# Optimization experiments

Hardware: AMD Instinct MI355X
Metric: run time of the kernel (lower is better)

## Reference

```python
import jax, jax.numpy as jnp
import numpy as np

GAMMA = 0.5
ITERATIONS = 1


def setup_inputs() -> dict:
    key = jax.random.key(0)
    # x: [batch, heads, num_windows, N, dim]
    x = jax.random.normal(key, (4, 8, 64, 256, 128), dtype=jnp.float32)
    return {"x": x}


def _l2norm(v):
    return v / jnp.linalg.norm(v, axis=-1, keepdims=True)


def _get_codebook(x):
    # x: [b,h,w,n,d] -> c: [b,h,w,d]
    B, H, W, N, D = x.shape
    c = _l2norm(jnp.sum(x, axis=-2))              # init: window mean direction
    xf = x.reshape(B, H, W * N, D)                # flatten windows: [b,h,l,d], l = W*N
    for _ in range(ITERATIONS):
        aff = jnp.einsum('bhnd,bhld->bhnl', c, xf)           # [b,h,W,W*N]
        a_hw = jax.nn.one_hot(jnp.argmax(aff, axis=-1), W * N, dtype=x.dtype)  # [b,h,W,W*N]
        a_n = jax.nn.one_hot(jnp.argmax(aff, axis=-2), W, dtype=x.dtype)       # [b,h,W*N,W]
        attn = a_hw + jnp.swapaxes(a_n, -2, -1)              # [b,h,W,W*N]
        delta_c = _l2norm(jnp.einsum('bhnl,bhld->bhnd', attn, xf))
        c = _l2norm(GAMMA * c + (1.0 - GAMMA) * delta_c)
    return c


def reference(x):
    # x: [b,h,w,n,d]
    W = x.shape[2]
    c = _get_codebook(x)                                     # [b,h,w,d]
    cos_sim = jnp.einsum('bhrcd,bhsd->bhrcs', x, c)          # [b,h,w,n,w]
    delta_onehot = jax.nn.one_hot(jnp.argmax(cos_sim, axis=-1), W, dtype=jnp.float32)
    return delta_onehot, c
```

## Files before the change

kernel.cpp:

```cpp
#include <hip/hip_runtime.h>

typedef unsigned long long u64;
typedef unsigned int u32;

#define G_ 32
#define L_ 16384
#define D_ 128
#define ONEHOT_ 33554432LL

__global__ __launch_bounds__(256) void k1_sums(const float* __restrict__ x,
                                               float* __restrict__ c0n) {
  int blk = blockIdx.x;
  const float* xp = x + ((size_t)blk << 15);
  int t = threadIdx.x;
  int d4 = t & 31, r0 = t >> 5;
  float4 acc = make_float4(0.f, 0.f, 0.f, 0.f);
  #pragma unroll 4
  for (int r = r0; r < 256; r += 8) {
    float4 v = *(const float4*)(xp + r * D_ + d4 * 4);
    acc.x += v.x; acc.y += v.y; acc.z += v.z; acc.w += v.w;
  }
  __shared__ float4 part[8][32];
  __shared__ double ssq[33];
  part[r0][d4] = acc;
  __syncthreads();
  if (t < 32) {
    float4 s = part[0][t];
    for (int r = 1; r < 8; ++r) {
      float4 v = part[r][t];
      s.x += v.x; s.y += v.y; s.z += v.z; s.w += v.w;
    }
    part[0][t] = s;
    ssq[t] = (double)s.x * s.x + (double)s.y * s.y + (double)s.z * s.z + (double)s.w * s.w;
  }
  __syncthreads();
  if (t == 0) {
    double tot = 0.0;
    for (int i = 0; i < 32; ++i) tot += ssq[i];
    ssq[32] = 1.0 / sqrt(tot);
  }
  __syncthreads();
  if (t < 32) {
    float rn = (float)ssq[32];
    float4 s = part[0][t];
    float4 c = make_float4(s.x * rn, s.y * rn, s.z * rn, s.w * rn);
    *(float4*)(c0n + ((size_t)blk << 7) + t * 4) = c;
  }
}

__global__ __launch_bounds__(512)
void k2_assign(const float* __restrict__ x,
               const float* __restrict__ c0n,
               u32* __restrict__ aPack,
               u64* __restrict__ best) {
  __shared__ float4 cL[64 * 33];
  __shared__ float4 xq[8][16 * 9];
  int g = blockIdx.x >> 4, bsub = blockIdx.x & 15;
  int t = threadIdx.x, lane = t & 63, wv = t >> 6;
  int l15 = lane & 15, pg = lane >> 4;
  const float* xg = x + ((size_t)g << 21);
  const float4* cg4 = (const float4*)(c0n + ((size_t)g << 13));
  for (int i = t; i < 2048; i += 512)
    cL[(i >> 5) * 33 + (i & 31)] = cg4[i];
  __syncthreads();

  float4* xw = xq[wv];
  int sp = lane >> 2, sh = lane & 3;

  float rbv[4]; int rbp[4];
  #pragma unroll
  for (int s = 0; s < 4; ++s) { rbv[s] = -3.0e38f; rbp[s] = 0; }

  int wbase = bsub * 1024 + wv * 128;
  for (int tile = 0; tile < 8; ++tile) {
    int p0 = wbase + tile * 16;
    float4 acc[4][4];
    #pragma unroll
    for (int s = 0; s < 4; ++s)
      #pragma unroll
      for (int j = 0; j < 4; ++j) acc[s][j] = make_float4(0.f, 0.f, 0.f, 0.f);

    for (int q = 0; q < 4; ++q) {
      const float4* gsrc = (const float4*)(xg + ((size_t)(p0 + sp) << 7) + (q << 5));
      float4* xrow = xw + sp * 9;
      xrow[sh * 2]     = gsrc[sh * 2];
      xrow[sh * 2 + 1] = gsrc[sh * 2 + 1];
      #pragma unroll
      for (int d4l = 0; d4l < 8; ++d4l) {
        float4 ca[4];
        #pragma unroll
        for (int s = 0; s < 4; ++s)
          ca[s] = cL[(l15 + (s << 4)) * 33 + (q << 3) + d4l];
        #pragma unroll
        for (int j = 0; j < 4; ++j) {
          float4 xv = xw[(pg * 4 + j) * 9 + d4l];
          #pragma unroll
          for (int s = 0; s < 4; ++s) {
            acc[s][j].x += ca[s].x * xv.x;
            acc[s][j].y += ca[s].y * xv.y;
            acc[s][j].z += ca[s].z * xv.z;
            acc[s][j].w += ca[s].w * xv.w;
          }
        }
      }
    }

    int w1s[4];
    #pragma unroll
    for (int j = 0; j < 4; ++j) {
      int p = p0 + pg * 4 + j;
      float av[4];
      #pragma unroll
      for (int s = 0; s < 4; ++s)
        av[s] = (acc[s][j].x + acc[s][j].y) + (acc[s][j].z + acc[s][j].w);
      #pragma unroll
      for (int s = 0; s < 4; ++s)
        if (av[s] > rbv[s]) { rbv[s] = av[s]; rbp[s] = p; }
      float v1 = av[0]; int w1 = l15;
      #pragma unroll
      for (int s = 1; s < 4; ++s)
        if (av[s] > v1) { v1 = av[s]; w1 = l15 + (s << 4); }
      #pragma unroll
      for (int off = 1; off <= 8; off <<= 1) {
        float ov = __shfl_xor(v1, off); int ow = __shfl_xor(w1, off);
        if (ov > v1 || (ov == v1 && ow < w1)) { v1 = ov; w1 = ow; }
      }
      w1s[j] = w1;
    }

    if (l15 == 0) {
      u32 pk4 = (u32)w1s[0] | ((u32)w1s[1] << 8) |
                ((u32)w1s[2] << 16) | ((u32)w1s[3] << 24);
      aPack[((g * L_ + p0) >> 2) + pg] = pk4;
    }
  }

  #pragma unroll
  for (int s = 0; s < 4; ++s) {
    #pragma unroll
    for (int off = 16; off <= 32; off <<= 1) {
      float ov = __shfl_xor(rbv[s], off); int op = __shfl_xor(rbp[s], off);
      if (ov > rbv[s] || (ov == rbv[s] && op < rbp[s])) { rbv[s] = ov; rbp[s] = op; }
    }
  }
  if (pg == 0) {
    #pragma unroll
    for (int s = 0; s < 4; ++s) {
      u32 key = __float_as_uint(rbv[s]);
      key ^= (key & 0x80000000u) ? 0xFFFFFFFFu : 0x80000000u;
      u64 pk = ((u64)key << 32) | (u64)(0xFFFFFFFFu - (u32)rbp[s]);
      atomicMax(&best[(g << 6) + l15 + (s << 4)], pk);
    }
  }
}

__global__ __launch_bounds__(1024)
void k2d_delta(const float* __restrict__ x,
               const u32* __restrict__ aPack,
               u64* __restrict__ deltaI) {
  __shared__ u64 ldsD[64 * 130];
  int g = blockIdx.x >> 3, bsub = blockIdx.x & 7;
  int t = threadIdx.x, lane = t & 63, wv = t >> 6;
  const float* xg = x + ((size_t)g << 21);
  for (int i = t; i < 64 * 130; i += 1024) ldsD[i] = 0ULL;
  __syncthreads();

  int pbase = bsub * 2048 + wv * 128;
  #pragma unroll 2
  for (int i4 = 0; i4 < 32; ++i4) {
    int p0 = pbase + i4 * 4;
    u32 pk4 = aPack[(g * L_ + p0) >> 2];
    #pragma unroll
    for (int j = 0; j < 4; ++j) {
      int aw = (int)((pk4 >> (j * 8)) & 63u);
      const float* xr = xg + ((size_t)(p0 + j) << 7);
      float va = xr[lane];
      float vb = xr[lane + 64];
      u64* dst = ldsD + aw * 130 + lane;
      atomicAdd(dst, (u64)(long long)__double2ll_rn((double)va * 4294967296.0));
      atomicAdd(dst + 64, (u64)(long long)__double2ll_rn((double)vb * 4294967296.0));
    }
  }

  __syncthreads();
  for (int i = t; i < 8192; i += 1024) {
    u64 v = ldsD[(i >> 7) * 130 + (i & 127)];
    if (v) atomicAdd(&deltaI[((size_t)g << 13) + i], v);
  }
}

__global__ __launch_bounds__(128) void k3_final(const float* __restrict__ x,
                                                const float* __restrict__ c0n,
                                                const u64* __restrict__ deltaI,
                                                const u64* __restrict__ best,
                                                float* __restrict__ cOut,
                                                float* __restrict__ c2n) {
  int blk = blockIdx.x, g = blk >> 6;
  int d = threadIdx.x;
  u64 pk = best[blk];
  int bl = (int)(0xFFFFFFFFu - (u32)(pk & 0xFFFFFFFFull));
  float xb = x[((size_t)g << 21) + ((size_t)bl << 7) + d];
  long long di = (long long)deltaI[((size_t)blk << 7) + d];
  double delta = (double)di * (1.0 / 4294967296.0) + (double)xb;

  __shared__ double red[128];
  __shared__ double inv;
  red[d] = delta * delta;
  __syncthreads();
  for (int s = 64; s > 0; s >>= 1) {
    if (d < s) red[d] += red[d + s];
    __syncthreads();
  }
  if (d == 0) inv = 1.0 / sqrt(red[0]);
  __syncthreads();
  float dn = (float)(delta * inv);
  float b2 = 0.5f * c0n[((size_t)blk << 7) + d] + 0.5f * dn;
  __syncthreads();
  red[d] = (double)b2 * b2;
  __syncthreads();
  for (int s = 64; s > 0; s >>= 1) {
    if (d < s) red[d] += red[d + s];
    __syncthreads();
  }
  if (d == 0) inv = 1.0 / sqrt(red[0]);
  __syncthreads();
  float cf = b2 * (float)inv;
  cOut[((size_t)blk << 7) + d] = cf;
  c2n[((size_t)blk << 7) + d] = cf;
}

__global__ __launch_bounds__(512)
void k4_onehot(const float* __restrict__ x,
               const float* __restrict__ c2n,
               float* __restrict__ out) {
  __shared__ float4 cL[64 * 33];
  __shared__ float4 xq[8][16 * 9];
  int g = blockIdx.x >> 4, bsub = blockIdx.x & 15;
  int t = threadIdx.x, lane = t & 63, wv = t >> 6;
  int l15 = lane & 15, pg = lane >> 4;
  const float* xg = x + ((size_t)g << 21);
  const float4* cg4 = (const float4*)(c2n + ((size_t)g << 13));
  for (int i = t; i < 2048; i += 512)
    cL[(i >> 5) * 33 + (i & 31)] = cg4[i];
  __syncthreads();

  float4* xw = xq[wv];
  int sp = lane >> 2, sh = lane & 3;

  int wbase = bsub * 1024 + wv * 128;
  for (int tile = 0; tile < 8; ++tile) {
    int p0 = wbase + tile * 16;
    float4 acc[4][4];
    #pragma unroll
    for (int s = 0; s < 4; ++s)
      #pragma unroll
      for (int j = 0; j < 4; ++j) acc[s][j] = make_float4(0.f, 0.f, 0.f, 0.f);

    for (int q = 0; q < 4; ++q) {
      const float4* gsrc = (const float4*)(xg + ((size_t)(p0 + sp) << 7) + (q << 5));
      float4* xrow = xw + sp * 9;
      xrow[sh * 2]     = gsrc[sh * 2];
      xrow[sh * 2 + 1] = gsrc[sh * 2 + 1];
      #pragma unroll
      for (int d4l = 0; d4l < 8; ++d4l) {
        float4 ca[4];
        #pragma unroll
        for (int s = 0; s < 4; ++s)
          ca[s] = cL[(l15 + (s << 4)) * 33 + (q << 3) + d4l];
        #pragma unroll
        for (int j = 0; j < 4; ++j) {
          float4 xv = xw[(pg * 4 + j) * 9 + d4l];
          #pragma unroll
          for (int s = 0; s < 4; ++s) {
            acc[s][j].x += ca[s].x * xv.x;
            acc[s][j].y += ca[s].y * xv.y;
            acc[s][j].z += ca[s].z * xv.z;
            acc[s][j].w += ca[s].w * xv.w;
          }
        }
      }
    }

    #pragma unroll
    for (int j = 0; j < 4; ++j) {
      int p = p0 + pg * 4 + j;
      float av[4];
      #pragma unroll
      for (int s = 0; s < 4; ++s)
        av[s] = (acc[s][j].x + acc[s][j].y) + (acc[s][j].z + acc[s][j].w);
      float v1 = av[0]; int w1 = l15;
      #pragma unroll
      for (int s = 1; s < 4; ++s)
        if (av[s] > v1) { v1 = av[s]; w1 = l15 + (s << 4); }
      #pragma unroll
      for (int off = 1; off <= 8; off <<= 1) {
        float ov = __shfl_xor(v1, off); int ow = __shfl_xor(w1, off);
        if (ov > v1 || (ov == v1 && ow < w1)) { v1 = ov; w1 = ow; }
      }
      int w0 = l15 << 2;
      float4 vv;
      vv.x = (w1 == w0    ) ? 1.f : 0.f;
      vv.y = (w1 == w0 + 1) ? 1.f : 0.f;
      vv.z = (w1 == w0 + 2) ? 1.f : 0.f;
      vv.w = (w1 == w0 + 3) ? 1.f : 0.f;
      *(float4*)(out + (((size_t)(g * L_ + p)) << 6) + w0) = vv;
    }
  }
}

extern "C" void kernel_launch(void* const* d_in, const int* in_sizes, int n_in,
                              void* d_out, int out_size, void* d_ws, size_t ws_size,
                              hipStream_t stream) {
  const float* x = (const float*)d_in[0];
  float* out = (float*)d_out;
  float* cOut = out + ONEHOT_;
  char* ws = (char*)d_ws;
  float* c0n   = (float*)(ws);
  float* c2n   = (float*)(ws + (1u << 20));
  u64*  deltaI = (u64*)(ws + (3u << 20));
  u64*  best   = (u64*)(ws + (5u << 20));
  u32*  aPack  = (u32*)(ws + (5u << 20) + 65536);

  hipMemsetAsync(ws + (3u << 20), 0, (2u << 20) + 16384, stream);

  hipLaunchKernelGGL(k1_sums,   dim3(2048), dim3(256),  0, stream, x, c0n);
  hipLaunchKernelGGL(k2_assign, dim3(512),  dim3(512),  0, stream, x, c0n, aPack, best);
  hipLaunchKernelGGL(k2d_delta, dim3(256),  dim3(1024), 0, stream, x, aPack, deltaI);
  hipLaunchKernelGGL(k3_final,  dim3(2048), dim3(128),  0, stream,
                     x, c0n, deltaI, best, cOut, c2n);
  hipLaunchKernelGGL(k4_onehot, dim3(512),  dim3(512),  0, stream, x, c2n, out);
}
```

Baseline: 485.4 us.

## Double-buffer x tiles with register prefetch and larger per-thread tile in onehot kernel

Restructures k4_onehot to use 4 waves of 256 threads, each processing 32 points per tile (8 per thread) instead of 16. The next x chunk is prefetched into registers while the current chunk is being consumed. LDS x buffers are double-buffered with an XOR swizzle to avoid bank conflicts. This aims to hide global load latency and raise arithmetic intensity per c load, at the cost of more accumulator registers (128 floats) and fewer threads per block.

After: 635.1 us. 30.8% more time.

```diff
diff --git a/kernel.cpp b/kernel.cpp
--- a/kernel.cpp
+++ b/kernel.cpp
@@ -229,38 +229,57 @@
   c2n[((size_t)blk << 7) + d] = cf;
 }
 
-__global__ __launch_bounds__(512)
+__global__ __launch_bounds__(256)
 void k4_onehot(const float* __restrict__ x,
                const float* __restrict__ c2n,
                float* __restrict__ out) {
   __shared__ float4 cL[64 * 33];
-  __shared__ float4 xq[8][16 * 9];
+  __shared__ float4 xq[4][2][256];
   int g = blockIdx.x >> 4, bsub = blockIdx.x & 15;
   int t = threadIdx.x, lane = t & 63, wv = t >> 6;
   int l15 = lane & 15, pg = lane >> 4;
   const float* xg = x + ((size_t)g << 21);
+  const float4* xg4 = (const float4*)xg;
   const float4* cg4 = (const float4*)(c2n + ((size_t)g << 13));
-  for (int i = t; i < 2048; i += 512)
+  for (int i = t; i < 2048; i += 256)
     cL[(i >> 5) * 33 + (i & 31)] = cg4[i];
   __syncthreads();
 
-  float4* xw = xq[wv];
-  int sp = lane >> 2, sh = lane & 3;
-
-  int wbase = bsub * 1024 + wv * 128;
+  int sp = lane >> 1, sh = lane & 1;
+  int wsw = (sp >> 3) << 1;
+  int rsw = pg << 1;
+  int wbase = bsub * 1024 + wv * 256;
+
+  float4 pr[4];
+  {
+    const float4* gp = xg4 + (size_t)(wbase + sp) * 32;
+    #pragma unroll
+    for (int i = 0; i < 4; ++i) pr[i] = gp[(sh << 2) + i];
+  }
+
   for (int tile = 0; tile < 8; ++tile) {
-    int p0 = wbase + tile * 16;
-    float4 acc[4][4];
+    int p0 = wbase + tile * 32;
+    float4 acc[4][8];
     #pragma unroll
     for (int s = 0; s < 4; ++s)
       #pragma unroll
-      for (int j = 0; j < 4; ++j) acc[s][j] = make_float4(0.f, 0.f, 0.f, 0.f);
+      for (int j = 0; j < 8; ++j) acc[s][j] = make_float4(0.f, 0.f, 0.f, 0.f);
 
     for (int q = 0; q < 4; ++q) {
-      const float4* gsrc = (const float4*)(xg + ((size_t)(p0 + sp) << 7) + (q << 5));
-      float4* xrow = xw + sp * 9;
-      xrow[sh * 2]     = gsrc[sh * 2];
-      xrow[sh * 2 + 1] = gsrc[sh * 2 + 1];
+      int qi = (tile << 2) + q;
+      float4* buf = &xq[wv][qi & 1][0];
+      #pragma unroll
+      for (int i = 0; i < 4; ++i) {
+        int d4l = (sh << 2) + i;
+        buf[sp * 8 + (d4l ^ wsw)] = pr[i];
+      }
+      if (qi < 31) {
+        int nq = qi + 1;
+        const float4* gp = xg4 +
+            (size_t)(wbase + ((nq >> 2) << 5) + sp) * 32 + ((nq & 3) << 3);
+        #pragma unroll
+        for (int i = 0; i < 4; ++i) pr[i] = gp[(sh << 2) + i];
+      }
       #pragma unroll
       for (int d4l = 0; d4l < 8; ++d4l) {
         float4 ca[4];
@@ -268,8 +287,8 @@
         for (int s = 0; s < 4; ++s)
           ca[s] = cL[(l15 + (s << 4)) * 33 + (q << 3) + d4l];
         #pragma unroll
-        for (int j = 0; j < 4; ++j) {
-          float4 xv = xw[(pg * 4 + j) * 9 + d4l];
+        for (int j = 0; j < 8; ++j) {
+          float4 xv = buf[((pg << 3) + j) * 8 + (d4l ^ rsw)];
           #pragma unroll
           for (int s = 0; s < 4; ++s) {
             acc[s][j].x += ca[s].x * xv.x;
@@ -282,8 +301,8 @@
     }
 
     #pragma unroll
-    for (int j = 0; j < 4; ++j) {
-      int p = p0 + pg * 4 + j;
+    for (int j = 0; j < 8; ++j) {
+      int p = p0 + (pg << 3) + j;
       float av[4];
       #pragma unroll
       for (int s = 0; s < 4; ++s)
@@ -328,5 +347,5 @@
   hipLaunchKernelGGL(k2d_delta, dim3(256),  dim3(1024), 0, stream, x, aPack, deltaI);
   hipLaunchKernelGGL(k3_final,  dim3(2048), dim3(128),  0, stream,
                      x, c0n, deltaI, best, cOut, c2n);
-  hipLaunchKernelGGL(k4_onehot, dim3(512),  dim3(512),  0, stream, x, c2n, out);
-}
+  hipLaunchKernelGGL(k4_onehot, dim3(512),  dim3(256),  0, stream, x, c2n, out);
+}
```
